# Kernel optimization log

Measured on AMD Instinct MI355X. Metric: run time of the kernel, lower is better.

## Reference

```python
import jax, jax.numpy as jnp
import numpy as np

NUM_HEADS = 16
DIM = 1024
B, L = 2, 2048
NEG = -10000000000.0


def setup_inputs() -> dict:
    key = jax.random.key(0)
    ks = jax.random.split(key, 8)
    queries = jax.random.normal(ks[0], (B, L, DIM), dtype=jnp.float32)
    keys = jax.random.normal(ks[1], (B, L, DIM), dtype=jnp.float32)
    values = jax.random.normal(ks[2], (B, L, DIM), dtype=jnp.float32)
    mask = jax.random.uniform(ks[3], (B, L, L)) < 0.1
    s = 1.0 / np.sqrt(DIM)
    Wq = jax.random.uniform(ks[4], (DIM, DIM), minval=-s, maxval=s, dtype=jnp.float32)
    Wk = jax.random.uniform(ks[5], (DIM, DIM), minval=-s, maxval=s, dtype=jnp.float32)
    Wv = jax.random.uniform(ks[6], (DIM, DIM), minval=-s, maxval=s, dtype=jnp.float32)
    Wo = jax.random.uniform(ks[7], (DIM, DIM), minval=-s, maxval=s, dtype=jnp.float32)
    return {"queries": queries, "keys": keys, "values": values, "mask": mask,
            "Wq": Wq, "Wk": Wk, "Wv": Wv, "Wo": Wo}


def reference(queries, keys, values, mask, Wq, Wk, Wv, Wo):
    b, l, d = queries.shape
    h = NUM_HEADS
    dk = d // h
    # torch Linear(bias=False): y = x @ W.T ; then view(b, l, dk, h) -> head axis LAST
    qs = (queries @ Wq.T).reshape(b, l, dk, h)
    ks = (keys @ Wk.T).reshape(b, l, dk, h)
    vs = (values @ Wv.T).reshape(b, l, dk, h)
    # routing is None in the live code path
    w = jnp.einsum('bidh,bodh->bioh', qs, ks) / jnp.sqrt(jnp.asarray(dk, jnp.float32))
    w = jnp.where(mask[..., None], NEG, w)          # masked_fill where mask True
    w = jax.nn.softmax(w, axis=-2)                   # softmax over key axis 'o'
    mha = jnp.einsum('bioh,bodh->bidh', w, vs).reshape(b, l, d)
    # dropout is identity in eval mode
    return mha @ Wo.T
```

## Files before the change

### kernel.cpp

```cpp
#include <hip/hip_runtime.h>
#include <hip/hip_bf16.h>
#include <cstdint>
#include <cstddef>

typedef unsigned short ushort_t;
typedef __attribute__((ext_vector_type(8))) short short8;
typedef __attribute__((ext_vector_type(8))) unsigned short ushort8;
typedef __attribute__((ext_vector_type(4))) unsigned short ushort4v;
typedef __attribute__((ext_vector_type(4))) float f32x4;
typedef __attribute__((ext_vector_type(2))) unsigned long long ull2;

#define LPAD 72

__device__ __forceinline__ unsigned short f2bf(float f) {
    unsigned int x = __float_as_uint(f);
    unsigned int r = x + 0x7fffu + ((x >> 16) & 1u);
    return (unsigned short)(r >> 16);
}

__device__ __forceinline__ void async16(const ushort_t* g, ushort_t* l) {
    __builtin_amdgcn_global_load_lds(
        (const __attribute__((address_space(1))) unsigned int*)g,
        (__attribute__((address_space(3))) unsigned int*)l,
        16, 0, 0);
}

__global__ __launch_bounds__(256) void cvt(const float* __restrict__ q,
                                           const float* __restrict__ k,
                                           const float* __restrict__ v,
                                           const float* __restrict__ Wq,
                                           const float* __restrict__ Wk,
                                           const float* __restrict__ Wv,
                                           ushort_t* __restrict__ qb,
                                           ushort_t* __restrict__ kb,
                                           ushort_t* __restrict__ vb,
                                           ushort_t* __restrict__ Wqb,
                                           ushort_t* __restrict__ Wkb,
                                           ushort_t* __restrict__ Wvb) {
    const int z = blockIdx.y;
    const float* X = (z == 0) ? q : (z == 1) ? k : v;
    const float* W = (z == 0) ? Wq : (z == 1) ? Wk : Wv;
    ushort_t* Xo = (z == 0) ? qb : (z == 1) ? kb : vb;
    ushort_t* Wo2 = (z == 0) ? Wqb : (z == 1) ? Wkb : Wvb;
    const size_t idx = (((size_t)blockIdx.x << 8) + threadIdx.x) << 3;
    const float* src; ushort_t* dst; float sc = 1.0f;
    if (idx < 4194304) { src = X + idx; dst = Xo + idx; if (z == 0) sc = 0.125f; }
    else               { src = W + (idx - 4194304); dst = Wo2 + (idx - 4194304); }
    f32x4 a0 = *(const f32x4*)src, a1 = *(const f32x4*)(src + 4);
    ushort8 o;
    #pragma unroll
    for (int j = 0; j < 4; j++) { o[j] = f2bf(a0[j] * sc); o[j + 4] = f2bf(a1[j] * sc); }
    *(ushort8*)dst = o;
}

__global__ __launch_bounds__(256) void maskbits_kernel(const int* __restrict__ mask,
                                                       unsigned long long* __restrict__ Mbits) {
    const int row  = blockIdx.x;
    const int w    = threadIdx.x >> 6;
    const int lane = threadIdx.x & 63;
    const int* mrow = mask + (size_t)row * 2048;
    #pragma unroll
    for (int it = 0; it < 8; it++) {
        const int o = (it << 8) + (w << 6) + lane;
        const unsigned long long bb = __ballot(mrow[o] != 0);
        if (lane == 0) Mbits[(size_t)((it << 2) + w) * 4096 + row] = bb;
    }
}

__global__ __launch_bounds__(256) void woswz(const float* __restrict__ W,
                                             ushort_t* __restrict__ WoH) {
    __shared__ float row[1024 + 64];
    const int j = blockIdx.x, t = threadIdx.x;
    f32x4 v = *(const f32x4*)(W + (size_t)j * 1024 + (t << 2));
    #pragma unroll
    for (int s = 0; s < 4; s++) { const int c = (t << 2) + s; row[c + (c >> 4)] = v[s]; }
    __syncthreads();
    #pragma unroll
    for (int s = 0; s < 4; s++) {
        const int k = t + (s << 8);
        const int col = ((k & 63) << 4) + (k >> 6);
        WoH[(size_t)j * 1024 + k] = f2bf(row[col + (col >> 4)]);
    }
}

__global__ __launch_bounds__(256) void gemm_proj(const ushort_t* __restrict__ qb,
                                                 const ushort_t* __restrict__ kb,
                                                 const ushort_t* __restrict__ vb,
                                                 const ushort_t* __restrict__ Wqb,
                                                 const ushort_t* __restrict__ Wkb,
                                                 const ushort_t* __restrict__ Wvb,
                                                 ushort_t* __restrict__ Qh,
                                                 ushort_t* __restrict__ Kh,
                                                 ushort_t* __restrict__ VhT) {
    __shared__ ushort_t Xs[512 * 8];
    __shared__ ushort_t Ws[512 * 8];

    const int lid  = blockIdx.x;
    const int nIdx = lid / 96;
    const int rem  = lid % 96;
    const int z    = rem >> 5;
    const int mIdx = rem & 31;
    const int n0   = nIdx << 7;
    const int m0   = mIdx << 7;

    const ushort_t* Xb = (z == 0) ? qb : (z == 1) ? kb : vb;
    const ushort_t* Wb = (z == 0) ? Wqb : (z == 1) ? Wkb : Wvb;

    const int tid  = threadIdx.x;
    const int w    = tid >> 6;
    const int lane = tid & 63;
    const int lm   = lane & 15;
    const int quad = lane >> 4;
    const int wm   = w & 1;
    const int wn   = w >> 1;

    f32x4 acc[4][4];
    #pragma unroll
    for (int i = 0; i < 4; i++)
        #pragma unroll
        for (int j = 0; j < 4; j++) acc[i][j] = (f32x4){0.f, 0.f, 0.f, 0.f};

    for (int k0 = 0; k0 < 1024; k0 += 32) {
        __syncthreads();
        #pragma unroll
        for (int i = 0; i < 2; i++) {
            const int L   = (((w << 1) + i) << 6) + lane;
            const int c4  = L >> 7, row = L & 127;
            const int lb  = (((w << 1) + i) << 6) << 3;
            async16(Xb + (size_t)(m0 + row) * 1024 + k0 + (c4 << 3), &Xs[lb]);
            async16(Wb + (size_t)(n0 + row) * 1024 + k0 + (c4 << 3), &Ws[lb]);
        }
        __syncthreads();
        short8 af[4], bf4[4];
        #pragma unroll
        for (int mf = 0; mf < 4; mf++)
            af[mf] = *(const short8*)&Xs[((quad << 7) + (wm << 6) + (mf << 4) + lm) << 3];
        #pragma unroll
        for (int nf = 0; nf < 4; nf++)
            bf4[nf] = *(const short8*)&Ws[((quad << 7) + (wn << 6) + (nf << 4) + lm) << 3];
        #pragma unroll
        for (int mf = 0; mf < 4; mf++)
            #pragma unroll
            for (int nf = 0; nf < 4; nf++)
                acc[mf][nf] = __builtin_amdgcn_mfma_f32_16x16x32_bf16(af[mf], bf4[nf], acc[mf][nf], 0, 0, 0);
    }

    const int bb    = m0 >> 11;
    const int l0    = m0 & 2047;
    const int dbase = (n0 >> 4) + (wn << 2);
    if (z != 2) {
        ushort_t* OUT = (z == 0) ? Qh : Kh;
        #pragma unroll
        for (int mf = 0; mf < 4; mf++)
            #pragma unroll
            for (int r = 0; r < 4; r++) {
                const int row = (wm << 6) + (mf << 4) + (quad << 2) + r;
                ushort4v o = { f2bf(acc[mf][0][r]), f2bf(acc[mf][1][r]),
                               f2bf(acc[mf][2][r]), f2bf(acc[mf][3][r]) };
                *(ushort4v*)(OUT + ((size_t)((bb << 4) + lm) * 2048 + l0 + row) * 64 + dbase) = o;
            }
    } else {
        #pragma unroll
        for (int mf = 0; mf < 4; mf++)
            #pragma unroll
            for (int nf = 0; nf < 4; nf++) {
                const int lbase = l0 + (wm << 6) + (mf << 4) + (quad << 2);
                ushort4v o = { f2bf(acc[mf][nf][0]), f2bf(acc[mf][nf][1]),
                               f2bf(acc[mf][nf][2]), f2bf(acc[mf][nf][3]) };
                *(ushort4v*)(VhT + ((size_t)((bb << 4) + lm) * 64 + dbase + nf) * 2048 + lbase) = o;
            }
    }
}

__global__ __launch_bounds__(256) void gemm_out(const ushort_t* __restrict__ mhaH,
                                                const ushort_t* __restrict__ WoH,
                                                float* __restrict__ C) {
    __shared__ ushort_t Xs[256 * 8];
    __shared__ ushort_t Ws[256 * 8];
    const int tid  = threadIdx.x;
    const int m0   = blockIdx.y << 6;
    const int n0   = blockIdx.x << 6;
    const int w    = tid >> 6;
    const int lane = tid & 63;
    const int lm   = lane & 15;
    const int quad = lane >> 4;
    const int ab   = m0 >> 11;
    const int al0  = m0 & 2047;

    f32x4 acc[4] = {{0.f,0.f,0.f,0.f},{0.f,0.f,0.f,0.f},{0.f,0.f,0.f,0.f},{0.f,0.f,0.f,0.f}};

    for (int k0 = 0; k0 < 1024; k0 += 32) {
        const int h  = k0 >> 6;
        const int d0 = k0 & 63;
        __syncthreads();
        async16(mhaH + (((size_t)(ab * 16 + h)) * 2048 + al0 + lane) * 64 + d0 + (w << 3),
                &Xs[(w << 6) << 3]);
        async16(WoH + (size_t)(n0 + lane) * 1024 + k0 + (w << 3),
                &Ws[(w << 6) << 3]);
        __syncthreads();
        short8 af = *(const short8*)&Xs[((quad << 6) + (w << 4) + lm) << 3];
        #pragma unroll
        for (int c = 0; c < 4; c++) {
            short8 bf = *(const short8*)&Ws[((quad << 6) + (c << 4) + lm) << 3];
            acc[c] = __builtin_amdgcn_mfma_f32_16x16x32_bf16(af, bf, acc[c], 0, 0, 0);
        }
    }
    #pragma unroll
    for (int c = 0; c < 4; c++) {
        #pragma unroll
        for (int r = 0; r < 4; r++) {
            const int row = m0 + (w << 4) + (quad << 2) + r;
            const int col = n0 + (c << 4) + lm;
            C[(size_t)row * 1024 + col] = acc[c][r];
        }
    }
}

__global__ __launch_bounds__(256, 2) void flash_attn(const ushort_t* __restrict__ Qh,
                                                     const ushort_t* __restrict__ Kh,
                                                     const ushort_t* __restrict__ VhT,
                                                     const unsigned long long* __restrict__ Mbits,
                                                     ushort_t* __restrict__ mhaH) {
    __shared__ ushort_t Ks[64 * LPAD];
    __shared__ ushort_t Vt[64 * LPAD];
    __shared__ ushort_t Pw[4][16 * LPAD];

    const int tid  = threadIdx.x;
    const int w    = tid >> 6;
    const int lane = tid & 63;
    const int lm   = lane & 15;
    const int quad = lane >> 4;
    const int bh   = blockIdx.y;
    const int b    = bh >> 4;
    const int q0   = blockIdx.x << 7;

    const ushort_t* Qb  = Qh  + ((size_t)bh << 17);
    const ushort_t* Kb  = Kh  + ((size_t)bh << 17);
    const ushort_t* Vtb = VhT + ((size_t)bh << 17);

    short8 aq[2][2];
    #pragma unroll
    for (int g = 0; g < 2; g++) {
        const ushort_t* qp = Qb + (size_t)(q0 + (w << 5) + (g << 4) + lm) * 64 + (quad << 3);
        aq[g][0] = *(const short8*)qp;
        aq[g][1] = *(const short8*)(qp + 32);
    }

    float l_part[2][4] = {{0.f,0.f,0.f,0.f},{0.f,0.f,0.f,0.f}};
    f32x4 o_acc[2][4] = {{{0.f,0.f,0.f,0.f},{0.f,0.f,0.f,0.f},{0.f,0.f,0.f,0.f},{0.f,0.f,0.f,0.f}},
                         {{0.f,0.f,0.f,0.f},{0.f,0.f,0.f,0.f},{0.f,0.f,0.f,0.f},{0.f,0.f,0.f,0.f}}};

    const int chunk0  = tid << 1;
    const int rowbase = (b << 11) + q0 + (w << 5);

    for (int kt0 = 0; kt0 < 2048; kt0 += 64) {
        __syncthreads();
        #pragma unroll
        for (int cc = 0; cc < 2; cc++) {
            const int chunk = chunk0 + cc;
            const int rr = chunk >> 3;
            const int rc = (chunk & 7) << 3;
            *(ushort8*)&Ks[rr * LPAD + rc] =
                *(const ushort8*)(Kb + (size_t)(kt0 + rr) * 64 + rc);
            *(ushort8*)&Vt[rr * LPAD + rc] =
                *(const ushort8*)(Vtb + (size_t)rr * 2048 + kt0 + rc);
        }
        __syncthreads();

        short8 bk[4][2], bv[4][2];
        #pragma unroll
        for (int c = 0; c < 4; c++) {
            bk[c][0] = *(const short8*)&Ks[((c << 4) + lm) * LPAD + (quad << 3)];
            bk[c][1] = *(const short8*)&Ks[((c << 4) + lm) * LPAD + 32 + (quad << 3)];
            bv[c][0] = *(const short8*)&Vt[((c << 4) + lm) * LPAD + (quad << 3)];
            bv[c][1] = *(const short8*)&Vt[((c << 4) + lm) * LPAD + 32 + (quad << 3)];
        }

        const unsigned long long* Mt = Mbits + (size_t)(kt0 >> 6) * 4096 + rowbase;

        #pragma unroll
        for (int g = 0; g < 2; g++) {
            f32x4 s[4];
            #pragma unroll
            for (int c = 0; c < 4; c++) {
                f32x4 zz = {0.f, 0.f, 0.f, 0.f};
                zz = __builtin_amdgcn_mfma_f32_16x16x32_bf16(aq[g][0], bk[c][0], zz, 0, 0, 0);
                zz = __builtin_amdgcn_mfma_f32_16x16x32_bf16(aq[g][1], bk[c][1], zz, 0, 0, 0);
                s[c] = zz;
            }
            unsigned long long mb[4];
            {
                const unsigned long long* mp = Mt + (g << 4) + (quad << 2);
                ull2 t0 = *(const ull2*)mp;
                ull2 t1 = *(const ull2*)(mp + 2);
                mb[0] = t0[0]; mb[1] = t0[1]; mb[2] = t1[0]; mb[3] = t1[1];
            }
            #pragma unroll
            for (int r = 0; r < 4; r++) {
                const unsigned lo = (unsigned)mb[r];
                const unsigned hi = (unsigned)(mb[r] >> 32);
                float lsum = 0.f;
                #pragma unroll
                for (int c = 0; c < 4; c++) {
                    const unsigned word = (c & 2) ? hi : lo;
                    const unsigned bit = (word >> (((c & 1) << 4) + lm)) & 1u;
                    const float p = bit ? 0.f : __expf(s[c][r]);
                    s[c][r] = p;
                    lsum += p;
                }
                l_part[g][r] += lsum;
            }
            #pragma unroll
            for (int c = 0; c < 4; c++)
                #pragma unroll
                for (int r = 0; r < 4; r++)
                    Pw[w][((quad << 2) + r) * LPAD + (c << 4) + lm] = f2bf(s[c][r]);

            short8 ap0 = *(const short8*)&Pw[w][lm * LPAD + (quad << 3)];
            short8 ap1 = *(const short8*)&Pw[w][lm * LPAD + 32 + (quad << 3)];
            #pragma unroll
            for (int cd = 0; cd < 4; cd++) {
                o_acc[g][cd] = __builtin_amdgcn_mfma_f32_16x16x32_bf16(ap0, bv[cd][0], o_acc[g][cd], 0, 0, 0);
                o_acc[g][cd] = __builtin_amdgcn_mfma_f32_16x16x32_bf16(ap1, bv[cd][1], o_acc[g][cd], 0, 0, 0);
            }
        }
    }

    #pragma unroll
    for (int g = 0; g < 2; g++) {
        #pragma unroll
        for (int r = 0; r < 4; r++) {
            float l = l_part[g][r];
            l += __shfl_xor(l, 1, 64);
            l += __shfl_xor(l, 2, 64);
            l += __shfl_xor(l, 4, 64);
            l += __shfl_xor(l, 8, 64);
            const float inv_l = 1.0f / l;
            const int i = q0 + (w << 5) + (g << 4) + (quad << 2) + r;
            ushort_t* orow = mhaH + (((size_t)bh * 2048 + i) << 6);
            #pragma unroll
            for (int cd = 0; cd < 4; cd++)
                orow[(cd << 4) + lm] = f2bf(o_acc[g][cd][r] * inv_l);
        }
    }
}

extern "C" void kernel_launch(void* const* d_in, const int* in_sizes, int n_in,
                              void* d_out, int out_size, void* d_ws, size_t ws_size,
                              hipStream_t stream) {
    const float* q    = (const float*)d_in[0];
    const float* k    = (const float*)d_in[1];
    const float* v    = (const float*)d_in[2];
    const int*   mask = (const int*)d_in[3];
    const float* Wq   = (const float*)d_in[4];
    const float* Wk   = (const float*)d_in[5];
    const float* Wv   = (const float*)d_in[6];
    const float* Wo   = (const float*)d_in[7];
    float* out = (float*)d_out;

    ushort_t* qb   = (ushort_t*)d_ws;
    ushort_t* kb   = qb  + 4194304;
    ushort_t* vb   = kb  + 4194304;
    ushort_t* Wqb  = vb  + 4194304;
    ushort_t* Wkb  = Wqb + 1048576;
    ushort_t* Wvb  = Wkb + 1048576;
    ushort_t* Qh   = Wvb + 1048576;
    ushort_t* Kh   = Qh  + 4194304;
    ushort_t* VhT  = Kh  + 4194304;
    ushort_t* mhaH = qb;
    ushort_t* WoH  = kb;
    unsigned long long* Mbits = (unsigned long long*)(kb + 1048576);

    dim3 gb(256);
    cvt<<<dim3(2560, 3), gb, 0, stream>>>(q, k, v, Wq, Wk, Wv, qb, kb, vb, Wqb, Wkb, Wvb);
    gemm_proj<<<dim3(768), gb, 0, stream>>>(qb, kb, vb, Wqb, Wkb, Wvb, Qh, Kh, VhT);
    maskbits_kernel<<<dim3(4096), gb, 0, stream>>>(mask, Mbits);
    woswz<<<dim3(1024), gb, 0, stream>>>(Wo, WoH);
    flash_attn<<<dim3(16, 32), gb, 0, stream>>>(Qh, Kh, VhT, Mbits, mhaH);
    gemm_out<<<dim3(16, 64), gb, 0, stream>>>(mhaH, WoH, out);
}
```

Before: 324.1 us.

## Enlarge output GEMM tiles, swizzle block order, async-load K/V tiles, pack bf16 conversion

gemm_out moves from 64x64 to 128x64 tiles on a 2x2 wave grid, so each wave issues 8 MFMAs per k-step instead of 4. Both gemm_out and flash_attn switch to a 1-D grid with a block-index swizzle meant to group related blocks on the same XCD for better L2 reuse. In flash_attn, K and V tiles are loaded with direct global-to-LDS async loads in an MFMA-friendly order, and key columns are permuted so each lane handles a mask nibble and can write P with packed v_cvt_pk_bf16_f32 stores. This cuts VGPR staging, shared-memory store instructions and conversion ALU work, but depends on the permuted index mapping staying consistent across mask bits, P and V.

```diff
diff --git a/kernel.cpp b/kernel.cpp
--- a/kernel.cpp
+++ b/kernel.cpp
@@ -9,6 +9,7 @@
 typedef __attribute__((ext_vector_type(4))) unsigned short ushort4v;
 typedef __attribute__((ext_vector_type(4))) float f32x4;
 typedef __attribute__((ext_vector_type(2))) unsigned long long ull2;
+typedef __attribute__((ext_vector_type(2))) unsigned int uint2v;
 
 #define LPAD 72
 
@@ -16,6 +17,12 @@
     unsigned int x = __float_as_uint(f);
     unsigned int r = x + 0x7fffu + ((x >> 16) & 1u);
     return (unsigned short)(r >> 16);
+}
+
+__device__ __forceinline__ unsigned int cvt_pk_bf16(float lo, float hi) {
+    unsigned int r;
+    asm("v_cvt_pk_bf16_f32 %0, %1, %2" : "=v"(r) : "v"(lo), "v"(hi));
+    return r;
 }
 
 __device__ __forceinline__ void async16(const ushort_t* g, ushort_t* l) {
@@ -175,45 +182,72 @@
 __global__ __launch_bounds__(256) void gemm_out(const ushort_t* __restrict__ mhaH,
                                                 const ushort_t* __restrict__ WoH,
                                                 float* __restrict__ C) {
-    __shared__ ushort_t Xs[256 * 8];
+    __shared__ ushort_t Xs[512 * 8];
     __shared__ ushort_t Ws[256 * 8];
+
+    const int lid  = blockIdx.x;
+    const int mIdx = ((lid & 7) << 2) | ((lid >> 3) & 3);
+    const int nIdx = lid >> 5;
+    const int m0   = mIdx << 7;
+    const int n0   = nIdx << 6;
+
     const int tid  = threadIdx.x;
-    const int m0   = blockIdx.y << 6;
-    const int n0   = blockIdx.x << 6;
     const int w    = tid >> 6;
     const int lane = tid & 63;
     const int lm   = lane & 15;
     const int quad = lane >> 4;
+    const int wm   = w & 1;
+    const int wn   = w >> 1;
     const int ab   = m0 >> 11;
     const int al0  = m0 & 2047;
 
-    f32x4 acc[4] = {{0.f,0.f,0.f,0.f},{0.f,0.f,0.f,0.f},{0.f,0.f,0.f,0.f},{0.f,0.f,0.f,0.f}};
+    f32x4 acc[4][2];
+    #pragma unroll
+    for (int i = 0; i < 4; i++)
+        #pragma unroll
+        for (int j = 0; j < 2; j++) acc[i][j] = (f32x4){0.f, 0.f, 0.f, 0.f};
 
     for (int k0 = 0; k0 < 1024; k0 += 32) {
         const int h  = k0 >> 6;
         const int d0 = k0 & 63;
         __syncthreads();
-        async16(mhaH + (((size_t)(ab * 16 + h)) * 2048 + al0 + lane) * 64 + d0 + (w << 3),
-                &Xs[(w << 6) << 3]);
-        async16(WoH + (size_t)(n0 + lane) * 1024 + k0 + (w << 3),
-                &Ws[(w << 6) << 3]);
-        __syncthreads();
-        short8 af = *(const short8*)&Xs[((quad << 6) + (w << 4) + lm) << 3];
-        #pragma unroll
-        for (int c = 0; c < 4; c++) {
-            short8 bf = *(const short8*)&Ws[((quad << 6) + (c << 4) + lm) << 3];
-            acc[c] = __builtin_amdgcn_mfma_f32_16x16x32_bf16(af, bf, acc[c], 0, 0, 0);
-        }
-    }
-    #pragma unroll
-    for (int c = 0; c < 4; c++) {
-        #pragma unroll
-        for (int r = 0; r < 4; r++) {
-            const int row = m0 + (w << 4) + (quad << 2) + r;
-            const int col = n0 + (c << 4) + lm;
-            C[(size_t)row * 1024 + col] = acc[c][r];
-        }
-    }
+        #pragma unroll
+        for (int i = 0; i < 2; i++) {
+            const int L   = (i << 8) + (w << 6) + lane;
+            const int c4  = L >> 7, row = L & 127;
+            async16(mhaH + ((size_t)(ab * 16 + h) * 2048 + al0 + row) * 64 + d0 + (c4 << 3),
+                    &Xs[((i << 8) + (w << 6)) << 3]);
+        }
+        {
+            const int L   = (w << 6) + lane;
+            const int c4  = L >> 6, row = L & 63;
+            async16(WoH + (size_t)(n0 + row) * 1024 + k0 + (c4 << 3),
+                    &Ws[(w << 6) << 3]);
+        }
+        __syncthreads();
+        short8 af[4], bf2[2];
+        #pragma unroll
+        for (int mf = 0; mf < 4; mf++)
+            af[mf] = *(const short8*)&Xs[((quad << 7) + (wm << 6) + (mf << 4) + lm) << 3];
+        #pragma unroll
+        for (int nf = 0; nf < 2; nf++)
+            bf2[nf] = *(const short8*)&Ws[((quad << 6) + (wn << 5) + (nf << 4) + lm) << 3];
+        #pragma unroll
+        for (int mf = 0; mf < 4; mf++)
+            #pragma unroll
+            for (int nf = 0; nf < 2; nf++)
+                acc[mf][nf] = __builtin_amdgcn_mfma_f32_16x16x32_bf16(af[mf], bf2[nf], acc[mf][nf], 0, 0, 0);
+    }
+    #pragma unroll
+    for (int mf = 0; mf < 4; mf++)
+        #pragma unroll
+        for (int nf = 0; nf < 2; nf++)
+            #pragma unroll
+            for (int r = 0; r < 4; r++) {
+                const int row = m0 + (wm << 6) + (mf << 4) + (quad << 2) + r;
+                const int col = n0 + (wn << 5) + (nf << 4) + lm;
+                C[(size_t)row * 1024 + col] = acc[mf][nf][r];
+            }
 }
 
 __global__ __launch_bounds__(256, 2) void flash_attn(const ushort_t* __restrict__ Qh,
@@ -221,8 +255,8 @@
                                                      const ushort_t* __restrict__ VhT,
                                                      const unsigned long long* __restrict__ Mbits,
                                                      ushort_t* __restrict__ mhaH) {
-    __shared__ ushort_t Ks[64 * LPAD];
-    __shared__ ushort_t Vt[64 * LPAD];
+    __shared__ ushort_t Ks[512 * 8];
+    __shared__ ushort_t Vs[512 * 8];
     __shared__ ushort_t Pw[4][16 * LPAD];
 
     const int tid  = threadIdx.x;
@@ -230,9 +264,10 @@
     const int lane = tid & 63;
     const int lm   = lane & 15;
     const int quad = lane >> 4;
-    const int bh   = blockIdx.y;
+    const int lid  = blockIdx.x;
+    const int bh   = ((lid & 7) << 2) | ((lid >> 3) & 3);
+    const int q0   = (lid >> 5) << 7;
     const int b    = bh >> 4;
-    const int q0   = blockIdx.x << 7;
 
     const ushort_t* Qb  = Qh  + ((size_t)bh << 17);
     const ushort_t* Kb  = Kh  + ((size_t)bh << 17);
@@ -250,30 +285,32 @@
     f32x4 o_acc[2][4] = {{{0.f,0.f,0.f,0.f},{0.f,0.f,0.f,0.f},{0.f,0.f,0.f,0.f},{0.f,0.f,0.f,0.f}},
                          {{0.f,0.f,0.f,0.f},{0.f,0.f,0.f,0.f},{0.f,0.f,0.f,0.f},{0.f,0.f,0.f,0.f}}};
 
-    const int chunk0  = tid << 1;
-    const int rowbase = (b << 11) + q0 + (w << 5);
+    const int rowbase  = (b << 11) + q0 + (w << 5);
+    const int shamt    = (lm & 7) << 2;
+    const bool hi_half = lm >= 8;
+
+    const ushort_t* ksrc = Kb  + (size_t)((lm << 2) + w) * 64 + (quad << 3);
+    const ushort_t* vsrc = Vtb + (size_t)((w << 4) + lm) * 2048 + (quad << 3);
+    ushort_t* kdst0 = &Ks[((w << 7)     ) << 3];
+    ushort_t* kdst1 = &Ks[((w << 7) + 64) << 3];
+    ushort_t* vdst0 = &Vs[((w << 7)     ) << 3];
+    ushort_t* vdst1 = &Vs[((w << 7) + 64) << 3];
 
     for (int kt0 = 0; kt0 < 2048; kt0 += 64) {
         __syncthreads();
-        #pragma unroll
-        for (int cc = 0; cc < 2; cc++) {
-            const int chunk = chunk0 + cc;
-            const int rr = chunk >> 3;
-            const int rc = (chunk & 7) << 3;
-            *(ushort8*)&Ks[rr * LPAD + rc] =
-                *(const ushort8*)(Kb + (size_t)(kt0 + rr) * 64 + rc);
-            *(ushort8*)&Vt[rr * LPAD + rc] =
-                *(const ushort8*)(Vtb + (size_t)rr * 2048 + kt0 + rc);
-        }
+        async16(ksrc + (size_t)kt0 * 64,      kdst0);
+        async16(ksrc + (size_t)kt0 * 64 + 32, kdst1);
+        async16(vsrc + kt0,      vdst0);
+        async16(vsrc + kt0 + 32, vdst1);
         __syncthreads();
 
         short8 bk[4][2], bv[4][2];
         #pragma unroll
         for (int c = 0; c < 4; c++) {
-            bk[c][0] = *(const short8*)&Ks[((c << 4) + lm) * LPAD + (quad << 3)];
-            bk[c][1] = *(const short8*)&Ks[((c << 4) + lm) * LPAD + 32 + (quad << 3)];
-            bv[c][0] = *(const short8*)&Vt[((c << 4) + lm) * LPAD + (quad << 3)];
-            bv[c][1] = *(const short8*)&Vt[((c << 4) + lm) * LPAD + 32 + (quad << 3)];
+            bk[c][0] = *(const short8*)&Ks[((c << 7) + lane) << 3];
+            bk[c][1] = *(const short8*)&Ks[((c << 7) + 64 + lane) << 3];
+            bv[c][0] = *(const short8*)&Vs[((c << 7) + lane) << 3];
+            bv[c][1] = *(const short8*)&Vs[((c << 7) + 64 + lane) << 3];
         }
 
         const unsigned long long* Mt = Mbits + (size_t)(kt0 >> 6) * 4096 + rowbase;
@@ -297,25 +334,19 @@
             }
             #pragma unroll
             for (int r = 0; r < 4; r++) {
-                const unsigned lo = (unsigned)mb[r];
-                const unsigned hi = (unsigned)(mb[r] >> 32);
-                float lsum = 0.f;
-                #pragma unroll
-                for (int c = 0; c < 4; c++) {
-                    const unsigned word = (c & 2) ? hi : lo;
-                    const unsigned bit = (word >> (((c & 1) << 4) + lm)) & 1u;
-                    const float p = bit ? 0.f : __expf(s[c][r]);
-                    s[c][r] = p;
-                    lsum += p;
-                }
-                l_part[g][r] += lsum;
-            }
-            #pragma unroll
-            for (int c = 0; c < 4; c++)
-                #pragma unroll
-                for (int r = 0; r < 4; r++)
-                    Pw[w][((quad << 2) + r) * LPAD + (c << 4) + lm] = f2bf(s[c][r]);
-
+                const unsigned long long m64 = mb[r];
+                const unsigned word = hi_half ? (unsigned)(m64 >> 32) : (unsigned)m64;
+                const unsigned nib  = (word >> shamt) & 0xFu;
+                float p0 = __expf(s[0][r]); if (nib & 1u) p0 = 0.f;
+                float p1 = __expf(s[1][r]); if (nib & 2u) p1 = 0.f;
+                float p2 = __expf(s[2][r]); if (nib & 4u) p2 = 0.f;
+                float p3 = __expf(s[3][r]); if (nib & 8u) p3 = 0.f;
+                l_part[g][r] += (p0 + p1) + (p2 + p3);
+                uint2v pv2;
+                pv2[0] = cvt_pk_bf16(p0, p1);
+                pv2[1] = cvt_pk_bf16(p2, p3);
+                *(uint2v*)&Pw[w][((quad << 2) + r) * LPAD + (lm << 2)] = pv2;
+            }
             short8 ap0 = *(const short8*)&Pw[w][lm * LPAD + (quad << 3)];
             short8 ap1 = *(const short8*)&Pw[w][lm * LPAD + 32 + (quad << 3)];
             #pragma unroll
@@ -376,6 +407,6 @@
     gemm_proj<<<dim3(768), gb, 0, stream>>>(qb, kb, vb, Wqb, Wkb, Wvb, Qh, Kh, VhT);
     maskbits_kernel<<<dim3(4096), gb, 0, stream>>>(mask, Mbits);
     woswz<<<dim3(1024), gb, 0, stream>>>(Wo, WoH);
-    flash_attn<<<dim3(16, 32), gb, 0, stream>>>(Qh, Kh, VhT, Mbits, mhaH);
-    gemm_out<<<dim3(16, 64), gb, 0, stream>>>(mhaH, WoH, out);
-}
+    flash_attn<<<dim3(512), gb, 0, stream>>>(Qh, Kh, VhT, Mbits, mhaH);
+    gemm_out<<<dim3(512), gb, 0, stream>>>(mhaH, WoH, out);
+}
```

New measurement: 310.2 us. -4.3%, faster.
